# Kernel tuning notes

Hardware: AMD Instinct MI355X
Metric: run time of the kernel (lower is better)

## Reference

```python
import jax, jax.numpy as jnp
import numpy as np
from jax import lax

K = 31  # neighborhood kernel size
HEADS = 4


def nat2d(x, qkv_w, qkv_b, rpb, proj_w, proj_b, heads=HEADS, k=K):
    """Neighborhood Attention 2D. x: (B,H,W,C) NHWC. Returns (B,H,W,C)."""
    B, H, W, C = x.shape
    dh = C // heads
    scale = dh ** -0.5
    K2 = k * k
    qkv = x @ qkv_w.T + qkv_b                      # (B,H,W,3C)
    qkv = qkv.reshape(B, H, W, 3, heads, dh)
    q, kk, v = qkv[..., 0, :, :], qkv[..., 1, :, :], qkv[..., 2, :, :]
    # neighborhood window start, clamped to image (NATTEN semantics)
    ri = jnp.clip(jnp.arange(H) - k // 2, 0, H - k)   # (H,)
    ci = jnp.clip(jnp.arange(W) - k // 2, 0, W - k)   # (W,)
    row_idx = ri[:, None] + jnp.arange(k)[None, :]    # (H,k)
    col_idx = ci[:, None] + jnp.arange(k)[None, :]    # (W,k)

    def gather(t):  # (B,H,W,heads,dh) -> (B,H,W,K2,heads,dh)
        g = t[:, row_idx]                  # (B,H,k,W,heads,dh)
        g = g[:, :, :, col_idx]            # (B,H,k,W,k,heads,dh)
        g = jnp.transpose(g, (0, 1, 3, 2, 4, 5, 6))
        return g.reshape(B, H, W, K2, heads, dh)

    kg = gather(kk)
    vg = gather(v)
    logits = jnp.einsum('bijhd,bijnhd->bijhn', q * scale, kg)  # (B,H,W,heads,K2)
    # relative position bias: rpb (heads, 2k-1, 2k-1), index = key - query + (k-1)
    rrel = row_idx - jnp.arange(H)[:, None] + (k - 1)  # (H,k)
    crel = col_idx - jnp.arange(W)[:, None] + (k - 1)  # (W,k)
    bias = rpb[:, rrel]                                # (heads,H,k,2k-1)
    bias = bias[:, :, :, crel]                         # (heads,H,k,W,k)
    bias = jnp.transpose(bias, (0, 1, 3, 2, 4)).reshape(heads, H, W, K2)
    logits = logits + jnp.transpose(bias, (1, 2, 0, 3))[None]
    attn = jax.nn.softmax(logits, axis=-1)
    out = jnp.einsum('bijhn,bijnhd->bijhd', attn, vg).reshape(B, H, W, C)
    return out @ proj_w.T + proj_b


def setup_inputs() -> dict:
    key = jax.random.key(0)
    ks = jax.random.split(key, 16)
    B, H, W, C = 1, 36, 36, 64
    s = 0.02
    inp = {
        'x': jax.random.normal(ks[0], (B, H * W, C), jnp.float32),
        'H': H, 'W': W,
        'qkv_w1': jax.random.normal(ks[1], (3 * C, C), jnp.float32) * s,
        'qkv_b1': jnp.zeros((3 * C,), jnp.float32),
        'rpb1': jax.random.normal(ks[2], (HEADS, 2 * K - 1, 2 * K - 1), jnp.float32) * s,
        'proj_w1': jax.random.normal(ks[3], (C, C), jnp.float32) * s,
        'proj_b1': jnp.zeros((C,), jnp.float32),
        'qkv_w2': jax.random.normal(ks[4], (3 * C, C), jnp.float32) * s,
        'qkv_b2': jnp.zeros((3 * C,), jnp.float32),
        'rpb2': jax.random.normal(ks[5], (HEADS, 2 * K - 1, 2 * K - 1), jnp.float32) * s,
        'proj_w2': jax.random.normal(ks[6], (C, C), jnp.float32) * s,
        'proj_b2': jnp.zeros((C,), jnp.float32),
        'dw_w': jax.random.normal(ks[7], (C, 1, 3, 3), jnp.float32) * s,
        'dw_b': jnp.zeros((C,), jnp.float32),
        'lin_w': jax.random.normal(ks[8], (C, C), jnp.float32) * s,
        'lin_b': jnp.zeros((C,), jnp.float32),
    }
    return inp


def reference(x, H, W, qkv_w1, qkv_b1, rpb1, proj_w1, proj_b1,
              qkv_w2, qkv_b2, rpb2, proj_w2, proj_b2,
              dw_w, dw_b, lin_w, lin_b):
    B, N, C = x.shape
    x_nhwc = x.reshape(B, H, W, C)
    x_nat = nat2d(x_nhwc, qkv_w1, qkv_b1, rpb1, proj_w1, proj_b1)
    x_nat = nat2d(x_nat, qkv_w2, qkv_b2, rpb2, proj_w2, proj_b2)
    x_bchw = jnp.transpose(x_nhwc, (0, 3, 1, 2))
    x_conv = lax.conv_general_dilated(
        x_bchw, dw_w, window_strides=(1, 1), padding=((1, 1), (1, 1)),
        feature_group_count=C,
        dimension_numbers=('NCHW', 'OIHW', 'NCHW')) + dw_b[None, :, None, None]
    out = jnp.transpose(x_nat, (0, 3, 1, 2)) + x_conv       # (B,C,H,W)
    out = out.reshape(B, C, H * W).transpose(0, 2, 1)        # (B,L,C)
    return out @ lin_w.T + lin_b
```

## Files before the change

### kernel.cpp

```cpp
#include <hip/hip_runtime.h>


namespace {

__device__ __forceinline__ int iclampi(int v, int lo, int hi) {
  return v < lo ? lo : (v > hi ? hi : v);
}

template <bool WITH_T>
__global__ __launch_bounds__(256) void qkv_fused(
    const float* __restrict__ xin, const float* __restrict__ w,
    const float* __restrict__ b, float* __restrict__ planes,
    const float* __restrict__ pw1, const float* __restrict__ pw2,
    const float* __restrict__ lw, float* __restrict__ wT) {
  const int bid = blockIdx.x;
  const int tid = threadIdx.x;
  if (WITH_T && bid >= 1008) {
    const int t = bid - 1008;
    const int m = t >> 4;
    const int idx = (t & 15) * 256 + tid;
    const float* src = m == 0 ? pw1 : (m == 1 ? pw2 : lw);
    wT[m * 4096 + (idx & 63) * 64 + (idx >> 6)] = src[idx];
    return;
  }
  __shared__ float xs[64][65];
  __shared__ float ws4[4][64];
  const int pg = bid % 21, rg = bid / 21;
  const int wv = tid >> 6, lane = tid & 63;
  const int n0 = pg * 64;
  const int base = n0 * 64;
  const int maxf = 82944 - base;
  const float* xb = xin + base;
#pragma unroll
  for (int t4 = 0; t4 < 4; ++t4) {
    const int fi = (tid + t4 * 256) * 4;
    float4 v = make_float4(0.f, 0.f, 0.f, 0.f);
    if (fi < maxf) v = *(const float4*)(xb + fi);
    const int p = fi >> 6, c = fi & 63;
    xs[p][c] = v.x; xs[p][c + 1] = v.y; xs[p][c + 2] = v.z; xs[p][c + 3] = v.w;
  }
  ws4[tid >> 6][tid & 63] = w[rg * 256 + tid];
  __syncthreads();
  const int r = rg * 4 + wv;
  float acc = b[r];
#pragma unroll
  for (int cc = 0; cc < 64; ++cc) acc += xs[lane][cc] * ws4[wv][cc];
  const int n = n0 + lane;
  if (n < 1296) planes[r * 1296 + n] = acc;
}

__global__ __launch_bounds__(256, 2) void nat_attn_part(
    const float* __restrict__ planes, const float* __restrict__ rpb,
    float* __restrict__ part) {
  __shared__ float lpart[4][16][35];
  __shared__ float qlds[4][2][16];

  const int tid = threadIdx.x;
  const int h = tid >> 6;
  const int lane = tid & 63;
  const int bid = blockIdx.x;
  const int tile = bid / 10;
  const int rem = bid - tile * 10;
  const int s = rem >> 1;
  const int pr = rem & 1;
  const int i0 = (tile / 18) * 2;
  const int j0 = (tile % 18) * 2;

  const int iq = i0 + pr;
  const int riq = iclampi(iq - 15, 0, 5);
  const int jqa = j0, jqb = j0 + 1;
  const int cja = iclampi(jqa - 15, 0, 5);
  const int cjb = iclampi(jqb - 15, 0, 5);

  const float* Qp = planes + (size_t)(h * 16) * 1296;
  const float4* Kp4 = (const float4*)(planes + (size_t)(64 + h * 16) * 1296);
  const float4* Vp4 = (const float4*)(planes + (size_t)(128 + h * 16) * 1296);

  if (lane < 32) {
    const int qq = lane >> 4, dd = lane & 15;
    const int nq = iq * 36 + (qq ? jqb : jqa);
    qlds[h][qq][dd] = Qp[dd * 1296 + nq] * 0.25f;
  }

  const int rr = lane / 9;
  const int cg = lane - rr * 9;
  const int krr = s * 7 + rr;
  const int rA = riq + krr;
  const bool act = (krr <= 30) && (rr < 7);
  const int rL = rA > 35 ? 35 : rA;
  const int rc9 = rL * 9 + cg;
  const int br = iclampi(rA - iq + 30, 0, 60);
  const float* rpbh = rpb + h * 3721 + br * 61;

  float dta[4] = {0.f, 0.f, 0.f, 0.f};
  float dtb[4] = {0.f, 0.f, 0.f, 0.f};
#pragma unroll
  for (int d = 0; d < 16; ++d) {
    const float4 k4 = Kp4[d * 324 + rc9];
    const float qa = qlds[h][0][d], qb = qlds[h][1][d];
    dta[0] += qa * k4.x; dta[1] += qa * k4.y; dta[2] += qa * k4.z; dta[3] += qa * k4.w;
    dtb[0] += qb * k4.x; dtb[1] += qb * k4.y; dtb[2] += qb * k4.z; dtb[3] += qb * k4.w;
  }

  float pa[4], pb_[4];
  float dena = 0.f, denb = 0.f;
#pragma unroll
  for (int j = 0; j < 4; ++j) {
    const int col = cg * 4 + j;
    const bool ina = act && (col >= cja) && (col <= cja + 30);
    const bool inb = act && (col >= cjb) && (col <= cjb + 30);
    const int bca = iclampi(col - jqa + 30, 0, 60);
    const int bcb = iclampi(col - jqb + 30, 0, 60);
    const float la = fminf(dta[j] + rpbh[bca], 25.f);
    const float lb = fminf(dtb[j] + rpbh[bcb], 25.f);
    pa[j] = ina ? __expf(la) : 0.f;
    pb_[j] = inb ? __expf(lb) : 0.f;
    dena += pa[j];
    denb += pb_[j];
  }

  float acca[16], accb[16];
#pragma unroll
  for (int d = 0; d < 16; ++d) {
    const float4 v4 = Vp4[d * 324 + rc9];
    acca[d] = pa[0] * v4.x + pa[1] * v4.y + pa[2] * v4.z + pa[3] * v4.w;
    accb[d] = pb_[0] * v4.x + pb_[1] * v4.y + pb_[2] * v4.z + pb_[3] * v4.w;
  }

#pragma unroll
  for (int d = 0; d < 16; ++d) {
    acca[d] += __shfl_xor(acca[d], 1);
    acca[d] += __shfl_xor(acca[d], 2);
    accb[d] += __shfl_xor(accb[d], 1);
    accb[d] += __shfl_xor(accb[d], 2);
  }
  dena += __shfl_xor(dena, 1);
  dena += __shfl_xor(dena, 2);
  denb += __shfl_xor(denb, 1);
  denb += __shfl_xor(denb, 2);

  if ((lane & 3) == 0) {
    const int row = lane >> 2;
#pragma unroll
    for (int d = 0; d < 16; ++d) {
      lpart[h][row][d] = acca[d];
      lpart[h][row][17 + d] = accb[d];
    }
    lpart[h][row][16] = dena;
    lpart[h][row][33] = denb;
  }

  float* wsout = part + ((size_t)bid * 4 + h) * 36;
  if (lane < 34) {
    float t0 = 0.f;
#pragma unroll
    for (int l = 0; l < 16; ++l) t0 += lpart[h][l][lane];
    wsout[lane] = t0;
  }
}

template <bool FINAL>
__global__ __launch_bounds__(256) void nat_combine(
    const float* __restrict__ part, const float* __restrict__ pwT,
    const float* __restrict__ pb, const float* __restrict__ x,
    const float* __restrict__ dww, const float* __restrict__ dwb,
    const float* __restrict__ linT, const float* __restrict__ lb,
    float* __restrict__ out) {
  __shared__ float att[4][64];
  __shared__ float y_lds[4][64];
  const int tid = threadIdx.x;
  const int q = tid >> 6, lane = tid & 63;
  const int tile = blockIdx.x;
  const int i0 = (tile / 18) * 2, j0 = (tile % 18) * 2;
  const int pr = q >> 1, qq = q & 1;
  const int iq = i0 + pr, jq = j0 + qq;
  const int n = iq * 36 + jq;

  const int hh = lane >> 4, dd = lane & 15;
  const float* pbase = part + (size_t)tile * 1440 + pr * 144 + hh * 36 + qq * 17;
  float num = 0.f, den = 0.f;
#pragma unroll
  for (int sp = 0; sp < 5; ++sp) {
    num += pbase[sp * 288 + dd];
    den += pbase[sp * 288 + 16];
  }
  att[q][lane] = num / den;
  __syncthreads();

  float a = pb[lane];
#pragma unroll
  for (int cc = 0; cc < 64; ++cc) a += att[q][cc] * pwT[cc * 64 + lane];

  if (!FINAL) {
    out[n * 64 + lane] = a;
  } else {
    float y = a + dwb[lane];
#pragma unroll
    for (int di = -1; di <= 1; ++di) {
#pragma unroll
      for (int dj = -1; dj <= 1; ++dj) {
        const int ii = iq + di, jj = jq + dj;
        if (ii >= 0 && ii < 36 && jj >= 0 && jj < 36)
          y += x[(ii * 36 + jj) * 64 + lane] * dww[lane * 9 + (di + 1) * 3 + (dj + 1)];
      }
    }
    y_lds[q][lane] = y;
    __syncthreads();
    float o = lb[lane];
#pragma unroll
    for (int cc = 0; cc < 64; ++cc) o += y_lds[q][cc] * linT[cc * 64 + lane];
    out[n * 64 + lane] = o;
  }
}

}

extern "C" void kernel_launch(void* const* d_in, const int* in_sizes, int n_in,
                              void* d_out, int out_size, void* d_ws, size_t ws_size,
                              hipStream_t stream) {
  const float* x       = (const float*)d_in[0];
  const float* qkv_w1  = (const float*)d_in[3];
  const float* qkv_b1  = (const float*)d_in[4];
  const float* rpb1    = (const float*)d_in[5];
  const float* proj_w1 = (const float*)d_in[6];
  const float* proj_b1 = (const float*)d_in[7];
  const float* qkv_w2  = (const float*)d_in[8];
  const float* qkv_b2  = (const float*)d_in[9];
  const float* rpb2    = (const float*)d_in[10];
  const float* proj_w2 = (const float*)d_in[11];
  const float* proj_b2 = (const float*)d_in[12];
  const float* dw_w    = (const float*)d_in[13];
  const float* dw_b    = (const float*)d_in[14];
  const float* lin_w   = (const float*)d_in[15];
  const float* lin_b   = (const float*)d_in[16];
  float* out = (float*)d_out;

  float* ws = (float*)d_ws;
  float* planes = ws;
  float* natA   = ws + 248832;
  float* partb  = natA + 82944;
  float* wT     = partb + 466560;
  float* pwT1 = wT;
  float* pwT2 = wT + 4096;
  float* linT = wT + 8192;

  qkv_fused<true><<<1056, 256, 0, stream>>>(x, qkv_w1, qkv_b1, planes,
                                            proj_w1, proj_w2, lin_w, wT);
  nat_attn_part<<<3240, 256, 0, stream>>>(planes, rpb1, partb);
  nat_combine<false><<<324, 256, 0, stream>>>(partb, pwT1, proj_b1, nullptr,
                                              nullptr, nullptr, nullptr, nullptr,
                                              natA);
  qkv_fused<false><<<1008, 256, 0, stream>>>(natA, qkv_w2, qkv_b2, planes,
                                             nullptr, nullptr, nullptr, nullptr);
  nat_attn_part<<<3240, 256, 0, stream>>>(planes, rpb2, partb);
  nat_combine<true><<<324, 256, 0, stream>>>(partb, pwT2, proj_b2, x,
                                             dw_w, dw_b, linT, lin_b, out);
}
```

Baseline: 149.5 us.

## Process 2x2 query block per attention block to share K/V loads

Each attention block now handles all four queries of a 2x2 tile instead of one query row, so each K/V float4 load serves four queries rather than two. Because adjacent query rows have overlapping windows, rows are split over a union range and validity is masked per query row, and the partial-output layout grows to 72 floats per head. The grid shrinks by half, which cuts redundant global loads and launch work but raises register pressure and lowers parallelism.

```diff
diff --git a/kernel.cpp b/kernel.cpp
--- a/kernel.cpp
+++ b/kernel.cpp
@@ -52,110 +52,150 @@
 __global__ __launch_bounds__(256, 2) void nat_attn_part(
     const float* __restrict__ planes, const float* __restrict__ rpb,
     float* __restrict__ part) {
-  __shared__ float lpart[4][16][35];
-  __shared__ float qlds[4][2][16];
+  __shared__ float lpart[4][16][69];
+  __shared__ float qlds[4][4][16];
 
   const int tid = threadIdx.x;
   const int h = tid >> 6;
   const int lane = tid & 63;
   const int bid = blockIdx.x;
-  const int tile = bid / 10;
-  const int rem = bid - tile * 10;
-  const int s = rem >> 1;
-  const int pr = rem & 1;
+  const int tile = bid / 5;
+  const int s = bid - tile * 5;
   const int i0 = (tile / 18) * 2;
   const int j0 = (tile % 18) * 2;
 
-  const int iq = i0 + pr;
-  const int riq = iclampi(iq - 15, 0, 5);
-  const int jqa = j0, jqb = j0 + 1;
-  const int cja = iclampi(jqa - 15, 0, 5);
-  const int cjb = iclampi(jqb - 15, 0, 5);
+  const int riq0 = iclampi(i0 - 15, 0, 5);
+  const int riq1 = iclampi(i0 - 14, 0, 5);
+  const int cj0 = iclampi(j0 - 15, 0, 5);
+  const int cj1 = iclampi(j0 - 14, 0, 5);
+  const int nRr = (riq1 + 30) - riq0;
 
   const float* Qp = planes + (size_t)(h * 16) * 1296;
   const float4* Kp4 = (const float4*)(planes + (size_t)(64 + h * 16) * 1296);
   const float4* Vp4 = (const float4*)(planes + (size_t)(128 + h * 16) * 1296);
 
-  if (lane < 32) {
+  {
     const int qq = lane >> 4, dd = lane & 15;
-    const int nq = iq * 36 + (qq ? jqb : jqa);
+    const int nq = (i0 + (qq >> 1)) * 36 + j0 + (qq & 1);
     qlds[h][qq][dd] = Qp[dd * 1296 + nq] * 0.25f;
   }
 
   const int rr = lane / 9;
   const int cg = lane - rr * 9;
   const int krr = s * 7 + rr;
-  const int rA = riq + krr;
-  const bool act = (krr <= 30) && (rr < 7);
+  const int rA = riq0 + krr;
+  const bool act = (krr <= nRr) && (rr < 7);
   const int rL = rA > 35 ? 35 : rA;
   const int rc9 = rL * 9 + cg;
-  const int br = iclampi(rA - iq + 30, 0, 60);
-  const float* rpbh = rpb + h * 3721 + br * 61;
-
-  float dta[4] = {0.f, 0.f, 0.f, 0.f};
-  float dtb[4] = {0.f, 0.f, 0.f, 0.f};
+  const bool rowok0 = act && (rA >= riq0) && (rA <= riq0 + 30);
+  const bool rowok1 = act && (rA >= riq1) && (rA <= riq1 + 30);
+  const int br0 = iclampi(rA - i0 + 30, 0, 60);
+  const int br1 = iclampi(rA - i0 + 29, 0, 60);
+  const float* rpb0 = rpb + h * 3721 + br0 * 61;
+  const float* rpb1 = rpb + h * 3721 + br1 * 61;
+
+  float dt0[4] = {0.f, 0.f, 0.f, 0.f};
+  float dt1[4] = {0.f, 0.f, 0.f, 0.f};
+  float dt2[4] = {0.f, 0.f, 0.f, 0.f};
+  float dt3[4] = {0.f, 0.f, 0.f, 0.f};
 #pragma unroll
   for (int d = 0; d < 16; ++d) {
     const float4 k4 = Kp4[d * 324 + rc9];
-    const float qa = qlds[h][0][d], qb = qlds[h][1][d];
-    dta[0] += qa * k4.x; dta[1] += qa * k4.y; dta[2] += qa * k4.z; dta[3] += qa * k4.w;
-    dtb[0] += qb * k4.x; dtb[1] += qb * k4.y; dtb[2] += qb * k4.z; dtb[3] += qb * k4.w;
-  }
-
-  float pa[4], pb_[4];
-  float dena = 0.f, denb = 0.f;
+    const float q0 = qlds[h][0][d], q1 = qlds[h][1][d];
+    const float q2 = qlds[h][2][d], q3 = qlds[h][3][d];
+    dt0[0] += q0 * k4.x; dt0[1] += q0 * k4.y; dt0[2] += q0 * k4.z; dt0[3] += q0 * k4.w;
+    dt1[0] += q1 * k4.x; dt1[1] += q1 * k4.y; dt1[2] += q1 * k4.z; dt1[3] += q1 * k4.w;
+    dt2[0] += q2 * k4.x; dt2[1] += q2 * k4.y; dt2[2] += q2 * k4.z; dt2[3] += q2 * k4.w;
+    dt3[0] += q3 * k4.x; dt3[1] += q3 * k4.y; dt3[2] += q3 * k4.z; dt3[3] += q3 * k4.w;
+  }
+
+  float p0[4], p1[4], p2[4], p3[4];
+  float den0 = 0.f, den1 = 0.f, den2 = 0.f, den3 = 0.f;
 #pragma unroll
   for (int j = 0; j < 4; ++j) {
     const int col = cg * 4 + j;
-    const bool ina = act && (col >= cja) && (col <= cja + 30);
-    const bool inb = act && (col >= cjb) && (col <= cjb + 30);
-    const int bca = iclampi(col - jqa + 30, 0, 60);
-    const int bcb = iclampi(col - jqb + 30, 0, 60);
-    const float la = fminf(dta[j] + rpbh[bca], 25.f);
-    const float lb = fminf(dtb[j] + rpbh[bcb], 25.f);
-    pa[j] = ina ? __expf(la) : 0.f;
-    pb_[j] = inb ? __expf(lb) : 0.f;
-    dena += pa[j];
-    denb += pb_[j];
-  }
-
-  float acca[16], accb[16];
-#pragma unroll
-  for (int d = 0; d < 16; ++d) {
-    const float4 v4 = Vp4[d * 324 + rc9];
-    acca[d] = pa[0] * v4.x + pa[1] * v4.y + pa[2] * v4.z + pa[3] * v4.w;
-    accb[d] = pb_[0] * v4.x + pb_[1] * v4.y + pb_[2] * v4.z + pb_[3] * v4.w;
-  }
-
-#pragma unroll
-  for (int d = 0; d < 16; ++d) {
-    acca[d] += __shfl_xor(acca[d], 1);
-    acca[d] += __shfl_xor(acca[d], 2);
-    accb[d] += __shfl_xor(accb[d], 1);
-    accb[d] += __shfl_xor(accb[d], 2);
-  }
-  dena += __shfl_xor(dena, 1);
-  dena += __shfl_xor(dena, 2);
-  denb += __shfl_xor(denb, 1);
-  denb += __shfl_xor(denb, 2);
-
+    const bool c0 = (col >= cj0) && (col <= cj0 + 30);
+    const bool c1 = (col >= cj1) && (col <= cj1 + 30);
+    const int bc0 = iclampi(col - j0 + 30, 0, 60);
+    const int bc1 = iclampi(col - j0 + 29, 0, 60);
+    const float b00 = rpb0[bc0], b01 = rpb0[bc1];
+    const float b10 = rpb1[bc0], b11 = rpb1[bc1];
+    p0[j] = (rowok0 && c0) ? __expf(fminf(dt0[j] + b00, 25.f)) : 0.f;
+    p1[j] = (rowok0 && c1) ? __expf(fminf(dt1[j] + b01, 25.f)) : 0.f;
+    p2[j] = (rowok1 && c0) ? __expf(fminf(dt2[j] + b10, 25.f)) : 0.f;
+    p3[j] = (rowok1 && c1) ? __expf(fminf(dt3[j] + b11, 25.f)) : 0.f;
+    den0 += p0[j]; den1 += p1[j]; den2 += p2[j]; den3 += p3[j];
+  }
+
+  den0 += __shfl_xor(den0, 1); den0 += __shfl_xor(den0, 2);
+  den1 += __shfl_xor(den1, 1); den1 += __shfl_xor(den1, 2);
+  den2 += __shfl_xor(den2, 1); den2 += __shfl_xor(den2, 2);
+  den3 += __shfl_xor(den3, 1); den3 += __shfl_xor(den3, 2);
   if ((lane & 3) == 0) {
     const int row = lane >> 2;
-#pragma unroll
-    for (int d = 0; d < 16; ++d) {
-      lpart[h][row][d] = acca[d];
-      lpart[h][row][17 + d] = accb[d];
-    }
-    lpart[h][row][16] = dena;
-    lpart[h][row][33] = denb;
-  }
-
-  float* wsout = part + ((size_t)bid * 4 + h) * 36;
-  if (lane < 34) {
+    lpart[h][row][16] = den0;
+    lpart[h][row][33] = den1;
+    lpart[h][row][50] = den2;
+    lpart[h][row][67] = den3;
+  }
+
+  {
+    float acA[16], acB[16];
+#pragma unroll
+    for (int d = 0; d < 16; ++d) {
+      const float4 v4 = Vp4[d * 324 + rc9];
+      acA[d] = p0[0] * v4.x + p0[1] * v4.y + p0[2] * v4.z + p0[3] * v4.w;
+      acB[d] = p1[0] * v4.x + p1[1] * v4.y + p1[2] * v4.z + p1[3] * v4.w;
+    }
+#pragma unroll
+    for (int d = 0; d < 16; ++d) {
+      acA[d] += __shfl_xor(acA[d], 1); acA[d] += __shfl_xor(acA[d], 2);
+      acB[d] += __shfl_xor(acB[d], 1); acB[d] += __shfl_xor(acB[d], 2);
+    }
+    if ((lane & 3) == 0) {
+      const int row = lane >> 2;
+#pragma unroll
+      for (int d = 0; d < 16; ++d) {
+        lpart[h][row][d] = acA[d];
+        lpart[h][row][17 + d] = acB[d];
+      }
+    }
+  }
+  {
+    float acA[16], acB[16];
+#pragma unroll
+    for (int d = 0; d < 16; ++d) {
+      const float4 v4 = Vp4[d * 324 + rc9];
+      acA[d] = p2[0] * v4.x + p2[1] * v4.y + p2[2] * v4.z + p2[3] * v4.w;
+      acB[d] = p3[0] * v4.x + p3[1] * v4.y + p3[2] * v4.z + p3[3] * v4.w;
+    }
+#pragma unroll
+    for (int d = 0; d < 16; ++d) {
+      acA[d] += __shfl_xor(acA[d], 1); acA[d] += __shfl_xor(acA[d], 2);
+      acB[d] += __shfl_xor(acB[d], 1); acB[d] += __shfl_xor(acB[d], 2);
+    }
+    if ((lane & 3) == 0) {
+      const int row = lane >> 2;
+#pragma unroll
+      for (int d = 0; d < 16; ++d) {
+        lpart[h][row][34 + d] = acA[d];
+        lpart[h][row][51 + d] = acB[d];
+      }
+    }
+  }
+
+  float* wsout = part + ((size_t)bid * 4 + h) * 72;
+  {
     float t0 = 0.f;
 #pragma unroll
     for (int l = 0; l < 16; ++l) t0 += lpart[h][l][lane];
     wsout[lane] = t0;
+    if (lane < 4) {
+      float t1 = 0.f;
+#pragma unroll
+      for (int l = 0; l < 16; ++l) t1 += lpart[h][l][lane + 64];
+      wsout[lane + 64] = t1;
+    }
   }
 }
 
@@ -172,12 +212,11 @@
   const int q = tid >> 6, lane = tid & 63;
   const int tile = blockIdx.x;
   const int i0 = (tile / 18) * 2, j0 = (tile % 18) * 2;
-  const int pr = q >> 1, qq = q & 1;
-  const int iq = i0 + pr, jq = j0 + qq;
+  const int iq = i0 + (q >> 1), jq = j0 + (q & 1);
   const int n = iq * 36 + jq;
 
   const int hh = lane >> 4, dd = lane & 15;
-  const float* pbase = part + (size_t)tile * 1440 + pr * 144 + hh * 36 + qq * 17;
+  const float* pbase = part + ((size_t)tile * 5 * 4 + hh) * 72 + q * 17;
   float num = 0.f, den = 0.f;
 #pragma unroll
   for (int sp = 0; sp < 5; ++sp) {
@@ -246,13 +285,13 @@
 
   qkv_fused<true><<<1056, 256, 0, stream>>>(x, qkv_w1, qkv_b1, planes,
                                             proj_w1, proj_w2, lin_w, wT);
-  nat_attn_part<<<3240, 256, 0, stream>>>(planes, rpb1, partb);
+  nat_attn_part<<<1620, 256, 0, stream>>>(planes, rpb1, partb);
   nat_combine<false><<<324, 256, 0, stream>>>(partb, pwT1, proj_b1, nullptr,
                                               nullptr, nullptr, nullptr, nullptr,
                                               natA);
   qkv_fused<false><<<1008, 256, 0, stream>>>(natA, qkv_w2, qkv_b2, planes,
                                              nullptr, nullptr, nullptr, nullptr);
-  nat_attn_part<<<3240, 256, 0, stream>>>(planes, rpb2, partb);
+  nat_attn_part<<<1620, 256, 0, stream>>>(planes, rpb2, partb);
   nat_combine<true><<<324, 256, 0, stream>>>(partb, pwT2, proj_b2, x,
                                              dw_w, dw_b, linT, lin_b, out);
 }
```

After: 150.6 us. Within noise of the previous version (+0.7%).
